# Kernel tuning notes

Hardware: AMD Instinct MI355X
Metric: run time of the kernel (lower is better)

Reference implementation:

```python
import jax, jax.numpy as jnp
import numpy as np

B, N, F, D, M, R, K, TOPR = 32, 1024, 10, 64, 4, 8, 20, 2
TAU = 1.0
BN_EPS = 1e-5


def setup_inputs() -> dict:
    key = jax.random.key(0)
    ks = jax.random.split(key, 20)
    s = 0.1
    p = {}
    p['data'] = jax.random.normal(ks[0], (B, N, F), jnp.float32)
    u = jnp.clip(jax.random.uniform(ks[1], (B, M), jnp.float32), 1e-6, 1.0 - 1e-6)
    p['gumbel_noise'] = -jnp.log(-jnp.log(u))
    p['W_cond'] = jax.random.normal(ks[2], (F, D), jnp.float32) * s
    p['b_cond'] = jnp.zeros((D,), jnp.float32)
    p['W_ap'] = jax.random.normal(ks[3], (D, D), jnp.float32) * s
    p['b_ap'] = jnp.zeros((D,), jnp.float32)
    p['W_av'] = jax.random.normal(ks[4], (D, 1), jnp.float32) * s
    p['W_r'] = jax.random.normal(ks[5], (D, M), jnp.float32) * s
    p['b_r'] = jnp.zeros((M,), jnp.float32)
    p['e_base'] = jax.random.normal(ks[6], (N, D), jnp.float32) * s
    p['lr_u'] = jax.random.normal(ks[7], (M, N, R), jnp.float32) * s
    p['lr_v'] = jax.random.normal(ks[8], (M, R, D), jnp.float32) * s
    p['W_gnn'] = jax.random.normal(ks[9], (F, D), jnp.float32) * s
    p['att_i'] = jax.random.normal(ks[10], (D,), jnp.float32) * s
    p['att_j'] = jax.random.normal(ks[11], (D,), jnp.float32) * s
    p['att_em_i'] = jax.random.normal(ks[12], (D,), jnp.float32) * s
    p['att_em_j'] = jax.random.normal(ks[13], (D,), jnp.float32) * s
    p['b_gnn'] = jnp.zeros((D,), jnp.float32)
    p['bn1_gamma'] = jnp.ones((D,), jnp.float32)
    p['bn1_beta'] = jnp.zeros((D,), jnp.float32)
    p['node_embed_table'] = jax.random.normal(ks[14], (N, D), jnp.float32) * s
    p['bn_out_gamma'] = jnp.ones((D,), jnp.float32)
    p['bn_out_beta'] = jnp.zeros((D,), jnp.float32)
    p['W_out'] = jax.random.normal(ks[15], (D, 1), jnp.float32) * s
    p['b_out'] = jnp.zeros((1,), jnp.float32)
    return p


def _nan(x):
    return jnp.nan_to_num(x, nan=0.0, posinf=1e4, neginf=-1e4)


def _bn(x, gamma, beta, axes):
    # BatchNorm1d in training mode: biased batch stats over `axes`.
    mu = x.mean(axes, keepdims=True)
    var = x.var(axes, keepdims=True)
    return (x - mu) * jax.lax.rsqrt(var + BN_EPS) * gamma + beta


def reference(data, gumbel_noise, W_cond, b_cond, W_ap, b_ap, W_av, W_r, b_r,
              e_base, lr_u, lr_v, W_gnn, att_i, att_j, att_em_i, att_em_j,
              b_gnn, bn1_gamma, bn1_beta, node_embed_table,
              bn_out_gamma, bn_out_beta, W_out, b_out):
    x_det = jax.lax.stop_gradient(data)                      # data.clone().detach()
    # --- condition attention pooling ---
    h_it = data @ W_cond + b_cond                            # [B,N,D]
    ah = jax.nn.leaky_relu(h_it @ W_ap + b_ap, 0.2)
    e_it = _nan((ah @ W_av)[..., 0])                         # [B,N]
    beta = jax.nn.softmax(e_it, axis=1)
    h_sys = jnp.sum(beta[..., None] * h_it, axis=1)          # [B,D]
    # --- gumbel top-k routing with straight-through ---
    pi_soft = jax.nn.softmax((h_sys @ W_r + b_r + gumbel_noise) / TAU, axis=-1)
    topv, topi = jax.lax.top_k(pi_soft, TOPR)
    pi_hard = jnp.sum(jax.nn.one_hot(topi, M, dtype=pi_soft.dtype) * topv[..., None], axis=1)
    pi_hard = pi_hard / jnp.maximum(pi_hard.sum(-1, keepdims=True), 1e-12)
    pi_t = jax.lax.stop_gradient(pi_hard - pi_soft) + pi_soft
    # --- low-rank expert prototypes -> mixed node embeddings ---
    proto = e_base[None] + jnp.einsum('mnr,mrd->mnd', lr_u, lr_v)    # [M,N,D]
    mixed = _nan(jnp.einsum('bm,mnd->bnd', pi_t, proto))             # [B,N,D]
    # --- dynamic top-k graph construction ---
    scores = _nan(jnp.einsum('bid,bjd->bij', mixed, mixed))          # [B,N,N]
    topk_vals, topk_idx = jax.lax.top_k(scores, K)                   # src nodes per dst: [B,N,K]
    topk_w = jax.nn.softmax(topk_vals, axis=-1)                      # edge weights
    # --- GAT-style layer with embedding-augmented keys, self loops re-added ---
    x_lin = x_det @ W_gnn                                            # [B,N,D]
    s_i = x_lin @ att_i + mixed @ att_em_i                           # [B,N]
    s_j = x_lin @ att_j + mixed @ att_em_j
    sj_nb = jnp.take_along_axis(s_j, topk_idx.reshape(B, N * K), axis=1).reshape(B, N, K)
    self_mask = topk_idx == jnp.arange(N)[None, :, None]             # remove_self_loops on topk edges
    alpha_nb = jnp.where(self_mask, -jnp.inf, jax.nn.leaky_relu(s_i[:, :, None] + sj_nb, 0.2))
    alpha_self = jax.nn.leaky_relu(s_i + s_j, 0.2)
    att = jax.nn.softmax(jnp.concatenate([alpha_nb, alpha_self[..., None]], axis=-1), axis=-1)
    w_nb = att[..., :K] * topk_w                                     # edge_weight modulation
    w_self = att[..., K]
    x_src = jnp.take_along_axis(x_lin, topk_idx.reshape(B, N * K)[..., None], axis=1).reshape(B, N, K, D)
    gnn = jnp.einsum('bnk,bnkd->bnd', w_nb, x_src) + w_self[..., None] * x_lin + b_gnn
    gnn = jax.nn.relu(_bn(gnn.reshape(B * N, D), bn1_gamma, bn1_beta, 0).reshape(B, N, D))
    # --- output head ---
    out = gnn * node_embed_table[None]                               # [B,N,D]
    out = jax.nn.relu(_bn(out, bn_out_gamma, bn_out_beta, (0, 1)))   # dropout = identity (eval)
    out = (out @ W_out + b_out).reshape(-1, N)                       # [B,N]
    return out, h_sys, pi_soft
```

## Files before the change

### kernel.cpp

```cpp
#include <hip/hip_runtime.h>
#include <math.h>

#define BB 32
#define NN 1024
#define FF 10
#define DD 64
#define MM 4
#define RR 8
#define KK 20
#define BNROWS (BB*NN)

#define OFF_HIT   0ull
#define OFF_XLIN  2097152ull
#define OFF_EIT   4194304ull
#define OFF_PIT   4227072ull
#define OFF_MIXED 4227200ull
#define OFF_SI    6324352ull
#define OFF_SJ    6357120ull
#define OFF_GNN   7700608ull
#define OFF_OUTP  9797760ull
#define OFF_STAT  11894912ull
#define OFF_SC    (OFF_STAT + 6464ull)

__device__ __forceinline__ float wave_sum(float v) {
    #pragma unroll
    for (int off = 32; off; off >>= 1) v += __shfl_xor(v, off);
    return v;
}
__device__ __forceinline__ float wave_max(float v) {
    #pragma unroll
    for (int off = 32; off; off >>= 1) v = fmaxf(v, __shfl_xor(v, off));
    return v;
}
__device__ __forceinline__ float lane_bcast(float v, int l) {
    return __int_as_float(__builtin_amdgcn_readlane(__float_as_int(v), l));
}

__global__ __launch_bounds__(256) void k_rows(
    const float* __restrict__ data, const float* __restrict__ W_cond,
    const float* __restrict__ b_cond, const float* __restrict__ W_ap,
    const float* __restrict__ b_ap, const float* __restrict__ W_av,
    const float* __restrict__ W_gnn,
    float* __restrict__ h_it, float* __restrict__ x_lin, float* __restrict__ e_it,
    float* __restrict__ stats)
{
    if (blockIdx.x < 26) {
        int idx = blockIdx.x * 256 + threadIdx.x;
        if (idx < 6432) stats[idx] = 0.f;
    }
    int w = threadIdx.x >> 6, lane = threadIdx.x & 63;
    int r = blockIdx.x * 4 + w;
    const float* dr = data + r * FF;
    float df[FF];
    #pragma unroll
    for (int f = 0; f < FF; f++) df[f] = dr[f];
    float h = b_cond[lane], x = 0.f;
    #pragma unroll
    for (int f = 0; f < FF; f++) {
        h = fmaf(df[f], W_cond[f * DD + lane], h);
        x = fmaf(df[f], W_gnn[f * DD + lane], x);
    }
    h_it[r * DD + lane] = h;
    x_lin[r * DD + lane] = x;
    float acc = b_ap[lane];
    #pragma unroll
    for (int e2 = 0; e2 < DD; e2++)
        acc = fmaf(lane_bcast(h, e2), W_ap[e2 * DD + lane], acc);
    float lr = acc > 0.f ? acc : 0.2f * acc;
    float ep = wave_sum(lr * W_av[lane]);
    if (lane == 0) e_it[r] = ep;
}

__global__ __launch_bounds__(256) void k_pool2(
    const float* __restrict__ e_it, const float* __restrict__ h_it,
    float* __restrict__ num, float* __restrict__ den)
{
    int w = threadIdx.x >> 6, lane = threadIdx.x & 63;
    int b = blockIdx.x >> 3, ch = blockIdx.x & 7;
    int base = b * NN + ch * 128 + w * 32;
    float acc = 0.f, dn = 0.f;
    #pragma unroll 4
    for (int i = 0; i < 32; i++) {
        float e = e_it[base + i];
        float wgt = expf(e);
        acc = fmaf(wgt, h_it[(size_t)(base + i) * DD + lane], acc);
        dn += wgt;
    }
    __shared__ float pa[4][DD];
    __shared__ float pd[4];
    pa[w][lane] = acc;
    if (lane == 0) pd[w] = dn;
    __syncthreads();
    if (w == 0) {
        float s = pa[0][lane] + pa[1][lane] + pa[2][lane] + pa[3][lane];
        atomicAdd(&num[b * DD + lane], s);
        if (lane == 0) atomicAdd(&den[b], pd[0] + pd[1] + pd[2] + pd[3]);
    }
}

__global__ void k_route(const float* __restrict__ num, const float* __restrict__ den,
                        const float* __restrict__ W_r, const float* __restrict__ b_r,
                        const float* __restrict__ gumbel,
                        float* __restrict__ h_sys, float* __restrict__ pi_soft,
                        float* __restrict__ pi_t)
{
    int tid = threadIdx.x;
    for (int i = tid; i < BB * DD; i += 256)
        h_sys[i] = num[i] / den[i >> 6];
    if (tid >= BB) return;
    int b = tid;
    float inv = 1.0f / den[b];
    float lg[MM];
    #pragma unroll
    for (int m = 0; m < MM; m++) lg[m] = b_r[m] + gumbel[b * MM + m];
    for (int d = 0; d < DD; d++) {
        float hv = num[b * DD + d] * inv;
        #pragma unroll
        for (int m = 0; m < MM; m++) lg[m] = fmaf(hv, W_r[d * MM + m], lg[m]);
    }
    float mx = fmaxf(fmaxf(lg[0], lg[1]), fmaxf(lg[2], lg[3]));
    float s = 0.f, p[MM];
    #pragma unroll
    for (int m = 0; m < MM; m++) { p[m] = expf(lg[m] - mx); s += p[m]; }
    #pragma unroll
    for (int m = 0; m < MM; m++) { p[m] /= s; pi_soft[b * MM + m] = p[m]; }
    int i1 = 0; float v1 = p[0];
    #pragma unroll
    for (int m = 1; m < MM; m++) if (p[m] > v1) { v1 = p[m]; i1 = m; }
    int i2 = -1; float v2 = -1.f;
    #pragma unroll
    for (int m = 0; m < MM; m++) if (m != i1 && p[m] > v2) { v2 = p[m]; i2 = m; }
    float norm = fmaxf(v1 + v2, 1e-12f);
    #pragma unroll
    for (int m = 0; m < MM; m++)
        pi_t[b * MM + m] = (m == i1 ? v1 : (m == i2 ? v2 : 0.f)) / norm;
}

__global__ __launch_bounds__(256) void k_mixed(
    const float* __restrict__ e_base, const float* __restrict__ lr_u,
    const float* __restrict__ lr_v, const float* __restrict__ pi_t,
    const float* __restrict__ x_lin,
    const float* __restrict__ att_i, const float* __restrict__ att_j,
    const float* __restrict__ att_em_i, const float* __restrict__ att_em_j,
    float* __restrict__ mixed, float* __restrict__ s_i, float* __restrict__ s_j)
{
    int w = threadIdx.x >> 6, lane = threadIdx.x & 63;
    int r = blockIdx.x * 4 + w;
    int b = r >> 10, n = r & 1023;
    float LR[MM];
    #pragma unroll
    for (int m = 0; m < MM; m++) {
        float a = 0.f;
        #pragma unroll
        for (int rr = 0; rr < RR; rr++)
            a = fmaf(lr_u[(m * NN + n) * RR + rr], lr_v[(m * RR + rr) * DD + lane], a);
        LR[m] = a;
    }
    float eb = e_base[n * DD + lane];
    float mx = 0.f;
    #pragma unroll
    for (int m = 0; m < MM; m++) mx = fmaf(pi_t[b * MM + m], eb + LR[m], mx);
    mixed[(size_t)r * DD + lane] = mx;
    float x = x_lin[(size_t)r * DD + lane];
    float r1 = wave_sum(x * att_i[lane] + mx * att_em_i[lane]);
    float r2 = wave_sum(x * att_j[lane] + mx * att_em_j[lane]);
    if (lane == 0) { s_i[r] = r1; s_j[r] = r2; }
}

__global__ __launch_bounds__(256) void k_score(
    const float* __restrict__ mixed_chunk, float* __restrict__ sc)
{
    __shared__ float As[32 * 132];
    __shared__ float Bs[32 * 132];
    int t = threadIdx.x;
    int bb = blockIdx.x >> 6;
    int rr = blockIdx.x & 63;
    int it = rr >> 3, jt = rr & 7;
    int i0 = it * 128, j0 = jt * 128;
    const float* mb = mixed_chunk + (size_t)bb * NN * DD;

    int tx = t & 15, ty = t >> 4;
    float acc[8][8];
    #pragma unroll
    for (int a = 0; a < 8; a++)
        #pragma unroll
        for (int bj = 0; bj < 8; bj++) acc[a][bj] = 0.f;

    int rowi[4], qi[4], swi[4];
    #pragma unroll
    for (int c = 0; c < 4; c++) {
        int id = t + c * 256;
        rowi[c] = (id & 15) | ((id >> 7) << 4);
        qi[c] = (id >> 4) & 7;
        swi[c] = ((rowi[c] & 4) << 4) | ((rowi[c] >> 3) << 2) | (rowi[c] & 3);
    }

    float4 pa[4], pb[4];
    #pragma unroll
    for (int c = 0; c < 4; c++) {
        pa[c] = *(const float4*)(mb + (size_t)(i0 + rowi[c]) * DD + qi[c] * 4);
        pb[c] = *(const float4*)(mb + (size_t)(j0 + rowi[c]) * DD + qi[c] * 4);
    }
    for (int hh = 0; hh < 2; hh++) {
        if (hh) __syncthreads();
        #pragma unroll
        for (int c = 0; c < 4; c++) {
            int pos = qi[c] * 4 * 132 + swi[c];
            As[pos] = pa[c].x; As[pos + 132] = pa[c].y; As[pos + 264] = pa[c].z; As[pos + 396] = pa[c].w;
            Bs[pos] = pb[c].x; Bs[pos + 132] = pb[c].y; Bs[pos + 264] = pb[c].z; Bs[pos + 396] = pb[c].w;
        }
        __syncthreads();
        if (hh == 0) {
            #pragma unroll
            for (int c = 0; c < 4; c++) {
                pa[c] = *(const float4*)(mb + (size_t)(i0 + rowi[c]) * DD + 32 + qi[c] * 4);
                pb[c] = *(const float4*)(mb + (size_t)(j0 + rowi[c]) * DD + 32 + qi[c] * 4);
            }
        }
        #pragma unroll 4
        for (int d = 0; d < 32; d++) {
            float4 a0 = *(const float4*)&As[d * 132 + ty * 4];
            float4 a1 = *(const float4*)&As[d * 132 + 64 + ty * 4];
            float4 b0 = *(const float4*)&Bs[d * 132 + tx * 4];
            float4 b1 = *(const float4*)&Bs[d * 132 + 64 + tx * 4];
            float av[8] = {a0.x, a0.y, a0.z, a0.w, a1.x, a1.y, a1.z, a1.w};
            float bv[8] = {b0.x, b0.y, b0.z, b0.w, b1.x, b1.y, b1.z, b1.w};
            #pragma unroll
            for (int a = 0; a < 8; a++)
                #pragma unroll
                for (int bj = 0; bj < 8; bj++)
                    acc[a][bj] = fmaf(av[a], bv[bj], acc[a][bj]);
        }
    }

    float* out = sc + ((size_t)bb * NN + i0 + ty * 8) * NN + j0 + tx * 8;
    #pragma unroll
    for (int a = 0; a < 8; a++) {
        float4 o0 = {acc[a][0], acc[a][1], acc[a][2], acc[a][3]};
        float4 o1 = {acc[a][4], acc[a][5], acc[a][6], acc[a][7]};
        *(float4*)(out + (size_t)a * NN) = o0;
        *(float4*)(out + (size_t)a * NN + 4) = o1;
    }
}

__global__ __launch_bounds__(256) void k_selgat(
    const float* __restrict__ sc, int b0,
    const float* __restrict__ x_lin, const float* __restrict__ s_i,
    const float* __restrict__ s_j, const float* __restrict__ b_gnn,
    float* __restrict__ gnn_pre, float* __restrict__ bstats)
{
    int w = threadIdx.x >> 6, lane = threadIdx.x & 63;
    int lr = blockIdx.x * 4 + w;
    int r = b0 * NN + lr;
    int b = r >> 10, n = r & 1023;
    const float* row = sc + (size_t)lr * NN;

    unsigned uk[16];
    #pragma unroll
    for (int c = 0; c < 4; c++) {
        float4 v = *(const float4*)(row + c * 256 + lane * 4);
        float vv[4] = {v.x, v.y, v.z, v.w};
        #pragma unroll
        for (int q = 0; q < 4; q++) {
            unsigned u = __float_as_uint(vv[q]);
            uk[c * 4 + q] = u ^ (((unsigned)((int)u >> 31)) | 0x80000000u);
        }
    }
    unsigned mx = uk[0];
    #pragma unroll
    for (int i = 1; i < 16; i++) mx = uk[i] > mx ? uk[i] : mx;
    unsigned sv = mx;
    #pragma unroll
    for (int blk = 2; blk <= 64; blk <<= 1) {
        #pragma unroll
        for (int dist = blk >> 1; dist >= 1; dist >>= 1) {
            unsigned pv = (unsigned)__shfl_xor((int)sv, dist);
            bool up = (lane & blk) == 0;
            bool upper = (lane & dist) == 0;
            bool g = sv > pv;
            sv = (((g == upper) == up)) ? sv : pv;
        }
    }
    unsigned tau = (unsigned)__shfl((int)sv, 19);

    __shared__ unsigned skey[4][64];
    __shared__ int sjj[4][64];
    int base = 0;
    #pragma unroll
    for (int s = 0; s < 16; s++) {
        bool q = uk[s] >= tau;
        unsigned long long m = __ballot(q);
        if (q) {
            int pos = base + __popcll(m & ((1ull << lane) - 1ull));
            if (pos < 64) {
                skey[w][pos] = uk[s];
                sjj[w][pos] = ((s >> 2) << 8) + lane * 4 + (s & 3);
            }
        }
        base += __popcll(m);
    }
    int C = base;

    float vk = -INFINITY; int ik = 0;
    if (C <= 64) {
        unsigned ck = 0u; int cj = 0x7FFFFFFF;
        if (lane < C) { ck = skey[w][lane]; cj = sjj[w][lane]; }
        if (C <= 32) {
            #pragma unroll
            for (int blk = 2; blk <= 32; blk <<= 1)
                #pragma unroll
                for (int dist = blk >> 1; dist >= 1; dist >>= 1) {
                    unsigned pk = (unsigned)__shfl_xor((int)ck, dist);
                    int pj = __shfl_xor(cj, dist);
                    bool up = (lane & blk) == 0;
                    bool upper = (lane & dist) == 0;
                    bool g = (ck > pk) || (ck == pk && cj < pj);
                    bool keep = ((g == upper) == up);
                    ck = keep ? ck : pk; cj = keep ? cj : pj;
                }
        } else {
            #pragma unroll
            for (int blk = 2; blk <= 64; blk <<= 1)
                #pragma unroll
                for (int dist = blk >> 1; dist >= 1; dist >>= 1) {
                    unsigned pk = (unsigned)__shfl_xor((int)ck, dist);
                    int pj = __shfl_xor(cj, dist);
                    bool up = (lane & blk) == 0;
                    bool upper = (lane & dist) == 0;
                    bool g = (ck > pk) || (ck == pk && cj < pj);
                    bool keep = ((g == upper) == up);
                    ck = keep ? ck : pk; cj = keep ? cj : pj;
                }
        }
        if (lane < KK) {
            unsigned u = (ck & 0x80000000u) ? (ck ^ 0x80000000u) : ~ck;
            vk = __uint_as_float(u);
            ik = cj;
        }
    } else {
        for (int k = 0; k < KK; k++) {
            unsigned bm = uk[0]; int bsl = 0;
            #pragma unroll
            for (int i = 1; i < 16; i++) if (uk[i] > bm) { bm = uk[i]; bsl = i; }
            unsigned wm = bm;
            #pragma unroll
            for (int off = 32; off; off >>= 1) {
                unsigned tt = (unsigned)__shfl_xor((int)wm, off);
                wm = tt > wm ? tt : wm;
            }
            unsigned long long ball = __ballot(bm == wm);
            int winner = (int)__builtin_ctzll(ball);
            int slotw = __shfl(bsl, winner);
            int jw = ((slotw >> 2) << 8) + winner * 4 + (slotw & 3);
            unsigned u2 = (wm & 0x80000000u) ? (wm ^ 0x80000000u) : ~wm;
            if (lane == k) { vk = __uint_as_float(u2); ik = jw; }
            if (lane == winner) uk[bsl] = 0u;
        }
    }

    float m1 = wave_max(vk);
    float ek = (lane < KK) ? expf(vk - m1) : 0.f;
    float s1v = wave_sum(ek);
    float wk = ek / s1v;
    float si = s_i[r], sjn = s_j[r];
    float a = -INFINITY;
    if (lane < KK) {
        float sjk = s_j[(b << 10) + ik];
        float t2 = si + sjk;
        a = (ik == n) ? -INFINITY : (t2 > 0.f ? t2 : 0.2f * t2);
    }
    float ts = si + sjn;
    float aself = ts > 0.f ? ts : 0.2f * ts;
    float am = wave_max(fmaxf(a, aself));
    float ea = (lane < KK && a != -INFINITY) ? expf(a - am) : 0.f;
    float es = expf(aself - am);
    float ssm = wave_sum(ea) + es;
    float wnb = (ea / ssm) * wk;
    float wself = es / ssm;
    float acc = b_gnn[lane] + wself * x_lin[(size_t)r * DD + lane];
    #pragma unroll
    for (int k = 0; k < KK; k++) {
        int jk = __shfl(ik, k);
        float wv = __shfl(wnb, k);
        acc = fmaf(wv, x_lin[((size_t)(b << 10) + jk) * DD + lane], acc);
    }
    gnn_pre[(size_t)r * DD + lane] = acc;

    __shared__ float ps[4][64], pq[4][64];
    ps[w][lane] = acc;
    pq[w][lane] = acc * acc;
    __syncthreads();
    if (w == 0) {
        float s = ps[0][lane] + ps[1][lane] + ps[2][lane] + ps[3][lane];
        float q2 = pq[0][lane] + pq[1][lane] + pq[2][lane] + pq[3][lane];
        float* bk = bstats + (size_t)(blockIdx.x & 31) * 128;
        atomicAdd(&bk[lane], s);
        atomicAdd(&bk[DD + lane], q2);
    }
}

__global__ __launch_bounds__(256) void k_bn1(
    const float* __restrict__ gnn_pre, float* __restrict__ stats,
    const float* __restrict__ bstats,
    const float* __restrict__ gamma, const float* __restrict__ beta,
    const float* __restrict__ net, float* __restrict__ out_pre)
{
    int tid = threadIdx.x;
    int d0 = (tid & 15) * 4;
    float mean4[4], rs4[4], bt4[4];
    #pragma unroll
    for (int k = 0; k < 4; k++) {
        float s = 0.f, q = 0.f;
        #pragma unroll 8
        for (int bk = 0; bk < 32; bk++) {
            s += bstats[bk * 128 + d0 + k];
            q += bstats[bk * 128 + 64 + d0 + k];
        }
        float mu = s * (1.0f / BNROWS);
        float var = q * (1.0f / BNROWS) - mu * mu;
        mean4[k] = mu;
        rs4[k] = rsqrtf(var + 1e-5f) * gamma[d0 + k];
        bt4[k] = beta[d0 + k];
    }
    float s4[4] = {0, 0, 0, 0}, q4[4] = {0, 0, 0, 0};
    size_t base4 = (size_t)blockIdx.x * 2048;
    #pragma unroll
    for (int i = 0; i < 8; i++) {
        size_t f4 = base4 + (size_t)i * 256 + tid;
        float4 v = ((const float4*)gnn_pre)[f4];
        int n = ((int)(f4 >> 4)) & 1023;
        float4 nv = ((const float4*)net)[(size_t)n * 16 + (tid & 15)];
        float vv[4] = {v.x, v.y, v.z, v.w};
        float nn2[4] = {nv.x, nv.y, nv.z, nv.w};
        float ov[4];
        #pragma unroll
        for (int k = 0; k < 4; k++) {
            float y = (vv[k] - mean4[k]) * rs4[k] + bt4[k];
            y = y > 0.f ? y : 0.f;
            float o = y * nn2[k];
            ov[k] = o;
            s4[k] += o;
            q4[k] = fmaf(o, o, q4[k]);
        }
        float4 o4 = {ov[0], ov[1], ov[2], ov[3]};
        ((float4*)out_pre)[f4] = o4;
    }
    __shared__ float4 ls[256], lq[256];
    ls[tid] = make_float4(s4[0], s4[1], s4[2], s4[3]);
    lq[tid] = make_float4(q4[0], q4[1], q4[2], q4[3]);
    __syncthreads();
    if (tid < 16) {
        float4 S = ls[tid], Q = lq[tid];
        #pragma unroll
        for (int rr = 1; rr < 16; rr++) {
            float4 a = ls[tid + 16 * rr], b = lq[tid + 16 * rr];
            S.x += a.x; S.y += a.y; S.z += a.z; S.w += a.w;
            Q.x += b.x; Q.y += b.y; Q.z += b.z; Q.w += b.w;
        }
        atomicAdd(&stats[128 + tid * 4 + 0], S.x);
        atomicAdd(&stats[128 + tid * 4 + 1], S.y);
        atomicAdd(&stats[128 + tid * 4 + 2], S.z);
        atomicAdd(&stats[128 + tid * 4 + 3], S.w);
        atomicAdd(&stats[192 + tid * 4 + 0], Q.x);
        atomicAdd(&stats[192 + tid * 4 + 1], Q.y);
        atomicAdd(&stats[192 + tid * 4 + 2], Q.z);
        atomicAdd(&stats[192 + tid * 4 + 3], Q.w);
    }
}

__global__ __launch_bounds__(256) void k_head(
    const float* __restrict__ out_pre, const float* __restrict__ stats,
    const float* __restrict__ gamma, const float* __restrict__ beta,
    const float* __restrict__ W_out, const float* __restrict__ b_out,
    float* __restrict__ out)
{
    int w = threadIdx.x >> 6, lane = threadIdx.x & 63;
    int r = blockIdx.x * 4 + w;
    float mean = stats[lane] * (1.0f / BNROWS);
    float var = stats[DD + lane] * (1.0f / BNROWS) - mean * mean;
    float rs = rsqrtf(var + 1e-5f);
    float y = (out_pre[(size_t)r * DD + lane] - mean) * rs * gamma[lane] + beta[lane];
    y = y > 0.f ? y : 0.f;
    float p = wave_sum(y * W_out[lane]);
    if (lane == 0) out[r] = p + b_out[0];
}

extern "C" void kernel_launch(void* const* d_in, const int* in_sizes, int n_in,
                              void* d_out, int out_size, void* d_ws, size_t ws_size,
                              hipStream_t stream)
{
    const float* data     = (const float*)d_in[0];
    const float* gumbel   = (const float*)d_in[1];
    const float* W_cond   = (const float*)d_in[2];
    const float* b_cond   = (const float*)d_in[3];
    const float* W_ap     = (const float*)d_in[4];
    const float* b_ap     = (const float*)d_in[5];
    const float* W_av     = (const float*)d_in[6];
    const float* W_r      = (const float*)d_in[7];
    const float* b_r      = (const float*)d_in[8];
    const float* e_base   = (const float*)d_in[9];
    const float* lr_u     = (const float*)d_in[10];
    const float* lr_v     = (const float*)d_in[11];
    const float* W_gnn    = (const float*)d_in[12];
    const float* att_i    = (const float*)d_in[13];
    const float* att_j    = (const float*)d_in[14];
    const float* att_em_i = (const float*)d_in[15];
    const float* att_em_j = (const float*)d_in[16];
    const float* b_gnn    = (const float*)d_in[17];
    const float* bn1_g    = (const float*)d_in[18];
    const float* bn1_b    = (const float*)d_in[19];
    const float* net      = (const float*)d_in[20];
    const float* bno_g    = (const float*)d_in[21];
    const float* bno_b    = (const float*)d_in[22];
    const float* W_out    = (const float*)d_in[23];
    const float* b_out    = (const float*)d_in[24];

    float* ws = (float*)d_ws;
    float* h_it   = ws + OFF_HIT;
    float* x_lin  = ws + OFF_XLIN;
    float* e_it   = ws + OFF_EIT;
    float* pi_t   = ws + OFF_PIT;
    float* mixed  = ws + OFF_MIXED;
    float* s_i    = ws + OFF_SI;
    float* s_j    = ws + OFF_SJ;
    float* gnn_pre = ws + OFF_GNN;
    float* out_pre = ws + OFF_OUTP;
    float* stats   = ws + OFF_STAT;
    float* bstats  = stats + 256;
    float* pnum    = stats + 4352;
    float* pden    = stats + 6400;

    float* out0    = (float*)d_out;
    float* h_sys   = out0 + BB * NN;
    float* pi_soft = out0 + BB * NN + BB * DD;

    k_rows<<<BNROWS / 4, 256, 0, stream>>>(data, W_cond, b_cond, W_ap, b_ap, W_av, W_gnn,
                                           h_it, x_lin, e_it, stats);
    k_pool2<<<BB * 8, 256, 0, stream>>>(e_it, h_it, pnum, pden);
    k_route<<<1, 256, 0, stream>>>(pnum, pden, W_r, b_r, gumbel, h_sys, pi_soft, pi_t);
    k_mixed<<<BNROWS / 4, 256, 0, stream>>>(e_base, lr_u, lr_v, pi_t, x_lin,
                                            att_i, att_j, att_em_i, att_em_j, mixed, s_i, s_j);

    size_t ws_floats = ws_size / 4;
    size_t avail = ws_floats > OFF_SC ? ws_floats - OFF_SC : 0;
    int cb = (int)(avail / (size_t)(NN * NN));
    if (cb > BB) cb = BB;
    float* sc = ws + OFF_SC;
    if (cb < 1) { cb = 2; sc = h_it; }
    for (int b0 = 0; b0 < BB; b0 += cb) {
        int c = (BB - b0) < cb ? (BB - b0) : cb;
        k_score<<<c * 64, 256, 0, stream>>>(mixed + (size_t)b0 * NN * DD, sc);
        k_selgat<<<c * 256, 256, 0, stream>>>(sc, b0, x_lin, s_i, s_j, b_gnn, gnn_pre, bstats);
    }

    k_bn1<<<256, 256, 0, stream>>>(gnn_pre, stats, bstats, bn1_g, bn1_b, net, out_pre);
    k_head<<<BNROWS / 4, 256, 0, stream>>>(out_pre, stats + 128, bno_g, bno_b, W_out, b_out, out0);
}
```

Measured before the change: 319.4 us.

## Replace bitonic sorts in top-k with radix-select threshold via ballots

```diff
diff --git a/kernel.cpp b/kernel.cpp
--- a/kernel.cpp
+++ b/kernel.cpp
@@ -269,19 +269,18 @@
     unsigned mx = uk[0];
     #pragma unroll
     for (int i = 1; i < 16; i++) mx = uk[i] > mx ? uk[i] : mx;
-    unsigned sv = mx;
-    #pragma unroll
-    for (int blk = 2; blk <= 64; blk <<= 1) {
-        #pragma unroll
-        for (int dist = blk >> 1; dist >= 1; dist >>= 1) {
-            unsigned pv = (unsigned)__shfl_xor((int)sv, dist);
-            bool up = (lane & blk) == 0;
-            bool upper = (lane & dist) == 0;
-            bool g = sv > pv;
-            sv = (((g == upper) == up)) ? sv : pv;
-        }
-    }
-    unsigned tau = (unsigned)__shfl((int)sv, 19);
+
+    unsigned tau = 0;
+    {
+        int need = KK;
+        for (int bb2 = 31; bb2 >= 0; --bb2) {
+            unsigned above = ~((2u << bb2) - 1u);
+            bool hit = ((mx & above) == tau) && ((mx >> bb2) & 1u);
+            int c1 = __popcll(__ballot(hit));
+            if (c1 >= need) tau |= (1u << bb2);
+            else need -= c1;
+        }
+    }
 
     __shared__ unsigned skey[4][64];
     __shared__ int sjj[4][64];
@@ -302,37 +301,39 @@
     int C = base;
 
     float vk = -INFINITY; int ik = 0;
+    bool issel = false;
     if (C <= 64) {
         unsigned ck = 0u; int cj = 0x7FFFFFFF;
         if (lane < C) { ck = skey[w][lane]; cj = sjj[w][lane]; }
-        if (C <= 32) {
-            #pragma unroll
-            for (int blk = 2; blk <= 32; blk <<= 1)
-                #pragma unroll
-                for (int dist = blk >> 1; dist >= 1; dist >>= 1) {
-                    unsigned pk = (unsigned)__shfl_xor((int)ck, dist);
-                    int pj = __shfl_xor(cj, dist);
-                    bool up = (lane & blk) == 0;
-                    bool upper = (lane & dist) == 0;
-                    bool g = (ck > pk) || (ck == pk && cj < pj);
-                    bool keep = ((g == upper) == up);
-                    ck = keep ? ck : pk; cj = keep ? cj : pj;
-                }
-        } else {
-            #pragma unroll
-            for (int blk = 2; blk <= 64; blk <<= 1)
-                #pragma unroll
-                for (int dist = blk >> 1; dist >= 1; dist >>= 1) {
-                    unsigned pk = (unsigned)__shfl_xor((int)ck, dist);
-                    int pj = __shfl_xor(cj, dist);
-                    bool up = (lane & blk) == 0;
-                    bool upper = (lane & dist) == 0;
-                    bool g = (ck > pk) || (ck == pk && cj < pj);
-                    bool keep = ((g == upper) == up);
-                    ck = keep ? ck : pk; cj = keep ? cj : pj;
-                }
-        }
-        if (lane < KK) {
+        unsigned tau2 = 0;
+        {
+            int need = KK;
+            for (int bb2 = 31; bb2 >= 0; --bb2) {
+                unsigned above = ~((2u << bb2) - 1u);
+                bool hit = ((ck & above) == tau2) && ((ck >> bb2) & 1u);
+                int c1 = __popcll(__ballot(hit));
+                if (c1 >= need) tau2 |= (1u << bb2);
+                else need -= c1;
+            }
+        }
+        bool isgt = ck > tau2;
+        int cntgt = __popcll(__ballot(isgt));
+        int needq = KK - cntgt;
+        bool iseq = (ck == tau2);
+        unsigned long long eqm = __ballot(iseq);
+        if (__popcll(eqm) > needq) {
+            unsigned pj = 0; int needs = needq;
+            for (int bb2 = 31; bb2 >= 0; --bb2) {
+                unsigned above = ~((2u << bb2) - 1u);
+                bool hit0 = iseq && (((unsigned)cj & above) == pj) && !(((unsigned)cj >> bb2) & 1u);
+                int c0 = __popcll(__ballot(hit0));
+                if (c0 >= needs) {  }
+                else { needs -= c0; pj |= (1u << bb2); }
+            }
+            iseq = iseq && ((unsigned)cj <= pj);
+        }
+        issel = isgt || iseq;
+        if (issel) {
             unsigned u = (ck & 0x80000000u) ? (ck ^ 0x80000000u) : ~ck;
             vk = __uint_as_float(u);
             ik = cj;
@@ -356,15 +357,16 @@
             if (lane == k) { vk = __uint_as_float(u2); ik = jw; }
             if (lane == winner) uk[bsl] = 0u;
         }
+        issel = (lane < KK);
     }
 
     float m1 = wave_max(vk);
-    float ek = (lane < KK) ? expf(vk - m1) : 0.f;
+    float ek = issel ? expf(vk - m1) : 0.f;
     float s1v = wave_sum(ek);
     float wk = ek / s1v;
     float si = s_i[r], sjn = s_j[r];
     float a = -INFINITY;
-    if (lane < KK) {
+    if (issel) {
         float sjk = s_j[(b << 10) + ik];
         float t2 = si + sjk;
         a = (ik == n) ? -INFINITY : (t2 > 0.f ? t2 : 0.2f * t2);
@@ -372,16 +374,19 @@
     float ts = si + sjn;
     float aself = ts > 0.f ? ts : 0.2f * ts;
     float am = wave_max(fmaxf(a, aself));
-    float ea = (lane < KK && a != -INFINITY) ? expf(a - am) : 0.f;
+    float ea = (issel && a != -INFINITY) ? expf(a - am) : 0.f;
     float es = expf(aself - am);
     float ssm = wave_sum(ea) + es;
     float wnb = (ea / ssm) * wk;
     float wself = es / ssm;
     float acc = b_gnn[lane] + wself * x_lin[(size_t)r * DD + lane];
-    #pragma unroll
+    unsigned long long selm = __ballot(issel);
+    #pragma unroll 1
     for (int k = 0; k < KK; k++) {
-        int jk = __shfl(ik, k);
-        float wv = __shfl(wnb, k);
+        int ln = (int)__builtin_ctzll(selm);
+        selm &= (selm - 1ull);
+        int jk = __builtin_amdgcn_readlane(ik, ln);
+        float wv = __int_as_float(__builtin_amdgcn_readlane(__float_as_int(wnb), ln));
         acc = fmaf(wv, x_lin[((size_t)(b << 10) + jk) * DD + lane], acc);
     }
     gnn_pre[(size_t)r * DD + lane] = acc;
```

Result: slower. 333.5 us (+4.4%).

## Fuse attention pooling and routing into row kernel with last-block reduction

Applied to the files above, without the earlier changes.

```diff
diff --git a/kernel.cpp b/kernel.cpp
--- a/kernel.cpp
+++ b/kernel.cpp
@@ -20,7 +20,7 @@
 #define OFF_GNN   7700608ull
 #define OFF_OUTP  9797760ull
 #define OFF_STAT  11894912ull
-#define OFF_SC    (OFF_STAT + 6464ull)
+#define OFF_SC    (OFF_STAT + 21008ull)
 
 __device__ __forceinline__ float wave_sum(float v) {
     #pragma unroll
@@ -40,16 +40,16 @@
     const float* __restrict__ data, const float* __restrict__ W_cond,
     const float* __restrict__ b_cond, const float* __restrict__ W_ap,
     const float* __restrict__ b_ap, const float* __restrict__ W_av,
-    const float* __restrict__ W_gnn,
-    float* __restrict__ h_it, float* __restrict__ x_lin, float* __restrict__ e_it,
-    float* __restrict__ stats)
-{
-    if (blockIdx.x < 26) {
-        int idx = blockIdx.x * 256 + threadIdx.x;
-        if (idx < 6432) stats[idx] = 0.f;
-    }
-    int w = threadIdx.x >> 6, lane = threadIdx.x & 63;
+    const float* __restrict__ W_gnn, const float* __restrict__ W_r,
+    const float* __restrict__ b_r, const float* __restrict__ gumbel,
+    float* __restrict__ x_lin,
+    float* pnumb, float* pdenb, unsigned* cnt,
+    float* __restrict__ h_sys, float* __restrict__ pi_soft, float* __restrict__ pi_t)
+{
+    int tid = threadIdx.x;
+    int w = tid >> 6, lane = tid & 63;
     int r = blockIdx.x * 4 + w;
+    int b = r >> 10;
     const float* dr = data + r * FF;
     float df[FF];
     #pragma unroll
@@ -60,61 +60,54 @@
         h = fmaf(df[f], W_cond[f * DD + lane], h);
         x = fmaf(df[f], W_gnn[f * DD + lane], x);
     }
-    h_it[r * DD + lane] = h;
-    x_lin[r * DD + lane] = x;
+    x_lin[(size_t)r * DD + lane] = x;
     float acc = b_ap[lane];
     #pragma unroll
     for (int e2 = 0; e2 < DD; e2++)
         acc = fmaf(lane_bcast(h, e2), W_ap[e2 * DD + lane], acc);
-    float lr = acc > 0.f ? acc : 0.2f * acc;
-    float ep = wave_sum(lr * W_av[lane]);
-    if (lane == 0) e_it[r] = ep;
-}
-
-__global__ __launch_bounds__(256) void k_pool2(
-    const float* __restrict__ e_it, const float* __restrict__ h_it,
-    float* __restrict__ num, float* __restrict__ den)
-{
-    int w = threadIdx.x >> 6, lane = threadIdx.x & 63;
-    int b = blockIdx.x >> 3, ch = blockIdx.x & 7;
-    int base = b * NN + ch * 128 + w * 32;
-    float acc = 0.f, dn = 0.f;
-    #pragma unroll 4
-    for (int i = 0; i < 32; i++) {
-        float e = e_it[base + i];
-        float wgt = expf(e);
-        acc = fmaf(wgt, h_it[(size_t)(base + i) * DD + lane], acc);
-        dn += wgt;
-    }
-    __shared__ float pa[4][DD];
-    __shared__ float pd[4];
-    pa[w][lane] = acc;
-    if (lane == 0) pd[w] = dn;
+    float lr2 = acc > 0.f ? acc : 0.2f * acc;
+    float ep = wave_sum(lr2 * W_av[lane]);
+    float wgt = expf(ep);
+    int bank = blockIdx.x & 7;
+    atomicAdd(&pnumb[bank * 2048 + b * 64 + lane], wgt * h);
+    if (lane == 0) atomicAdd(&pdenb[bank * 32 + b], wgt);
+
+    __shared__ int is_last;
     __syncthreads();
-    if (w == 0) {
-        float s = pa[0][lane] + pa[1][lane] + pa[2][lane] + pa[3][lane];
-        atomicAdd(&num[b * DD + lane], s);
-        if (lane == 0) atomicAdd(&den[b], pd[0] + pd[1] + pd[2] + pd[3]);
-    }
-}
-
-__global__ void k_route(const float* __restrict__ num, const float* __restrict__ den,
-                        const float* __restrict__ W_r, const float* __restrict__ b_r,
-                        const float* __restrict__ gumbel,
-                        float* __restrict__ h_sys, float* __restrict__ pi_soft,
-                        float* __restrict__ pi_t)
-{
-    int tid = threadIdx.x;
-    for (int i = tid; i < BB * DD; i += 256)
-        h_sys[i] = num[i] / den[i >> 6];
+    if (tid == 0) {
+        __threadfence();
+        unsigned old = atomicAdd(cnt, 1u);
+        is_last = (old == (unsigned)(gridDim.x - 1)) ? 1 : 0;
+    }
+    __syncthreads();
+    if (!is_last) return;
+    __threadfence();
+
+    __shared__ float den_s[BB];
+    if (tid < BB) {
+        float d2 = 0.f;
+        #pragma unroll
+        for (int bk = 0; bk < 8; bk++) d2 += pdenb[bk * 32 + tid];
+        den_s[tid] = d2;
+    }
+    __syncthreads();
+    for (int i = tid; i < BB * DD; i += 256) {
+        float s = 0.f;
+        #pragma unroll
+        for (int bk = 0; bk < 8; bk++) s += pnumb[bk * 2048 + i];
+        h_sys[i] = s / den_s[i >> 6];
+    }
     if (tid >= BB) return;
-    int b = tid;
-    float inv = 1.0f / den[b];
+    int bb = tid;
+    float inv = 1.0f / den_s[bb];
     float lg[MM];
     #pragma unroll
-    for (int m = 0; m < MM; m++) lg[m] = b_r[m] + gumbel[b * MM + m];
+    for (int m = 0; m < MM; m++) lg[m] = b_r[m] + gumbel[bb * MM + m];
     for (int d = 0; d < DD; d++) {
-        float hv = num[b * DD + d] * inv;
+        float s = 0.f;
+        #pragma unroll
+        for (int bk = 0; bk < 8; bk++) s += pnumb[bk * 2048 + bb * 64 + d];
+        float hv = s * inv;
         #pragma unroll
         for (int m = 0; m < MM; m++) lg[m] = fmaf(hv, W_r[d * MM + m], lg[m]);
     }
@@ -123,7 +116,7 @@
     #pragma unroll
     for (int m = 0; m < MM; m++) { p[m] = expf(lg[m] - mx); s += p[m]; }
     #pragma unroll
-    for (int m = 0; m < MM; m++) { p[m] /= s; pi_soft[b * MM + m] = p[m]; }
+    for (int m = 0; m < MM; m++) { p[m] /= s; pi_soft[bb * MM + m] = p[m]; }
     int i1 = 0; float v1 = p[0];
     #pragma unroll
     for (int m = 1; m < MM; m++) if (p[m] > v1) { v1 = p[m]; i1 = m; }
@@ -133,7 +126,7 @@
     float norm = fmaxf(v1 + v2, 1e-12f);
     #pragma unroll
     for (int m = 0; m < MM; m++)
-        pi_t[b * MM + m] = (m == i1 ? v1 : (m == i2 ? v2 : 0.f)) / norm;
+        pi_t[bb * MM + m] = (m == i1 ? v1 : (m == i2 ? v2 : 0.f)) / norm;
 }
 
 __global__ __launch_bounds__(256) void k_mixed(
@@ -516,10 +509,8 @@
     const float* b_out    = (const float*)d_in[24];
 
     float* ws = (float*)d_ws;
-    float* h_it   = ws + OFF_HIT;
     float* x_lin  = ws + OFF_XLIN;
-    float* e_it   = ws + OFF_EIT;
-    float* pi_t   = ws + OFF_PIT;
+    float* pi_tb  = ws + OFF_PIT;
     float* mixed  = ws + OFF_MIXED;
     float* s_i    = ws + OFF_SI;
     float* s_j    = ws + OFF_SJ;
@@ -527,18 +518,20 @@
     float* out_pre = ws + OFF_OUTP;
     float* stats   = ws + OFF_STAT;
     float* bstats  = stats + 256;
-    float* pnum    = stats + 4352;
-    float* pden    = stats + 6400;
+    float* pnumb   = stats + 4352;
+    float* pdenb   = stats + 20736;
+    unsigned* cnt  = (unsigned*)(stats + 20992);
 
     float* out0    = (float*)d_out;
     float* h_sys   = out0 + BB * NN;
     float* pi_soft = out0 + BB * NN + BB * DD;
 
+    hipMemsetAsync(stats, 0, 21000 * sizeof(float), stream);
+
     k_rows<<<BNROWS / 4, 256, 0, stream>>>(data, W_cond, b_cond, W_ap, b_ap, W_av, W_gnn,
-                                           h_it, x_lin, e_it, stats);
-    k_pool2<<<BB * 8, 256, 0, stream>>>(e_it, h_it, pnum, pden);
-    k_route<<<1, 256, 0, stream>>>(pnum, pden, W_r, b_r, gumbel, h_sys, pi_soft, pi_t);
-    k_mixed<<<BNROWS / 4, 256, 0, stream>>>(e_base, lr_u, lr_v, pi_t, x_lin,
+                                           W_r, b_r, gumbel, x_lin,
+                                           pnumb, pdenb, cnt, h_sys, pi_soft, pi_tb);
+    k_mixed<<<BNROWS / 4, 256, 0, stream>>>(e_base, lr_u, lr_v, pi_tb, x_lin,
                                             att_i, att_j, att_em_i, att_em_j, mixed, s_i, s_j);
 
     size_t ws_floats = ws_size / 4;
@@ -546,7 +539,7 @@
     int cb = (int)(avail / (size_t)(NN * NN));
     if (cb > BB) cb = BB;
     float* sc = ws + OFF_SC;
-    if (cb < 1) { cb = 2; sc = h_it; }
+    if (cb < 1) { cb = 2; sc = ws + OFF_HIT; }
     for (int b0 = 0; b0 < BB; b0 += cb) {
         int c = (BB - b0) < cb ? (BB - b0) : cb;
         k_score<<<c * 64, 256, 0, stream>>>(mixed + (size_t)b0 * NN * DD, sc);
```

Result: slower. 490.4 us (+53.5%).

## Retile score GEMM to 32x256 tiles with A rows read directly from global

Applied to the files above, without the earlier changes.

```diff
diff --git a/kernel.cpp b/kernel.cpp
--- a/kernel.cpp
+++ b/kernel.cpp
@@ -170,77 +170,69 @@
 __global__ __launch_bounds__(256) void k_score(
     const float* __restrict__ mixed_chunk, float* __restrict__ sc)
 {
-    __shared__ float As[32 * 132];
-    __shared__ float Bs[32 * 132];
+    __shared__ float BT[32 * 264];
     int t = threadIdx.x;
-    int bb = blockIdx.x >> 6;
-    int rr = blockIdx.x & 63;
-    int it = rr >> 3, jt = rr & 7;
-    int i0 = it * 128, j0 = jt * 128;
+    int w = t >> 6, lane = t & 63;
+    int bb = blockIdx.x >> 7;
+    int rr = blockIdx.x & 127;
+    int it = rr >> 2, jt = rr & 3;
+    int i0 = it * 32, j0 = jt * 256;
     const float* mb = mixed_chunk + (size_t)bb * NN * DD;
-
-    int tx = t & 15, ty = t >> 4;
-    float acc[8][8];
-    #pragma unroll
-    for (int a = 0; a < 8; a++)
-        #pragma unroll
-        for (int bj = 0; bj < 8; bj++) acc[a][bj] = 0.f;
-
-    int rowi[4], qi[4], swi[4];
-    #pragma unroll
-    for (int c = 0; c < 4; c++) {
-        int id = t + c * 256;
-        rowi[c] = (id & 15) | ((id >> 7) << 4);
-        qi[c] = (id >> 4) & 7;
-        swi[c] = ((rowi[c] & 4) << 4) | ((rowi[c] >> 3) << 2) | (rowi[c] & 3);
-    }
-
-    float4 pa[4], pb[4];
-    #pragma unroll
-    for (int c = 0; c < 4; c++) {
-        pa[c] = *(const float4*)(mb + (size_t)(i0 + rowi[c]) * DD + qi[c] * 4);
-        pb[c] = *(const float4*)(mb + (size_t)(j0 + rowi[c]) * DD + qi[c] * 4);
+    const float* arow = mb + (size_t)(i0 + w * 8) * DD;
+
+    float4 acc4[8];
+    #pragma unroll
+    for (int a = 0; a < 8; a++) acc4[a] = make_float4(0.f, 0.f, 0.f, 0.f);
+
+    float4 pf[8];
+    {
+        const float* src = mb + (size_t)(j0 + t) * DD;
+        #pragma unroll
+        for (int i = 0; i < 8; i++) pf[i] = *(const float4*)(src + i * 4);
     }
     for (int hh = 0; hh < 2; hh++) {
         if (hh) __syncthreads();
         #pragma unroll
-        for (int c = 0; c < 4; c++) {
-            int pos = qi[c] * 4 * 132 + swi[c];
-            As[pos] = pa[c].x; As[pos + 132] = pa[c].y; As[pos + 264] = pa[c].z; As[pos + 396] = pa[c].w;
-            Bs[pos] = pb[c].x; Bs[pos + 132] = pb[c].y; Bs[pos + 264] = pb[c].z; Bs[pos + 396] = pb[c].w;
+        for (int i = 0; i < 8; i++) {
+            float4 v = pf[i];
+            int d0 = i * 4;
+            BT[(d0 + 0) * 264 + t] = v.x;
+            BT[(d0 + 1) * 264 + t] = v.y;
+            BT[(d0 + 2) * 264 + t] = v.z;
+            BT[(d0 + 3) * 264 + t] = v.w;
         }
         __syncthreads();
         if (hh == 0) {
-            #pragma unroll
-            for (int c = 0; c < 4; c++) {
-                pa[c] = *(const float4*)(mb + (size_t)(i0 + rowi[c]) * DD + 32 + qi[c] * 4);
-                pb[c] = *(const float4*)(mb + (size_t)(j0 + rowi[c]) * DD + 32 + qi[c] * 4);
+            const float* src = mb + (size_t)(j0 + t) * DD + 32;
+            #pragma unroll
+            for (int i = 0; i < 8; i++) pf[i] = *(const float4*)(src + i * 4);
+        }
+        int dh = hh * 32;
+        #pragma unroll 2
+        for (int d4 = 0; d4 < 8; d4++) {
+            float4 av[8];
+            #pragma unroll
+            for (int a = 0; a < 8; a++)
+                av[a] = *(const float4*)(arow + (size_t)a * DD + dh + d4 * 4);
+            #pragma unroll
+            for (int dd = 0; dd < 4; dd++) {
+                float4 bv = *(const float4*)&BT[(d4 * 4 + dd) * 264 + lane * 4];
+                #pragma unroll
+                for (int a = 0; a < 8; a++) {
+                    float as = dd == 0 ? av[a].x : dd == 1 ? av[a].y : dd == 2 ? av[a].z : av[a].w;
+                    acc4[a].x = fmaf(as, bv.x, acc4[a].x);
+                    acc4[a].y = fmaf(as, bv.y, acc4[a].y);
+                    acc4[a].z = fmaf(as, bv.z, acc4[a].z);
+                    acc4[a].w = fmaf(as, bv.w, acc4[a].w);
+                }
             }
         }
-        #pragma unroll 4
-        for (int d = 0; d < 32; d++) {
-            float4 a0 = *(const float4*)&As[d * 132 + ty * 4];
-            float4 a1 = *(const float4*)&As[d * 132 + 64 + ty * 4];
-            float4 b0 = *(const float4*)&Bs[d * 132 + tx * 4];
-            float4 b1 = *(const float4*)&Bs[d * 132 + 64 + tx * 4];
-            float av[8] = {a0.x, a0.y, a0.z, a0.w, a1.x, a1.y, a1.z, a1.w};
-            float bv[8] = {b0.x, b0.y, b0.z, b0.w, b1.x, b1.y, b1.z, b1.w};
-            #pragma unroll
-            for (int a = 0; a < 8; a++)
-                #pragma unroll
-                for (int bj = 0; bj < 8; bj++)
-                    acc[a][bj] = fmaf(av[a], bv[bj], acc[a][bj]);
-        }
-    }
-
-    float* out = sc + ((size_t)bb * NN + i0 + ty * 8) * NN + j0 + tx * 8;
-    #pragma unroll
-    for (int a = 0; a < 8; a++) {
-        float4 o0 = {acc[a][0], acc[a][1], acc[a][2], acc[a][3]};
-        float4 o1 = {acc[a][4], acc[a][5], acc[a][6], acc[a][7]};
-        *(float4*)(out + (size_t)a * NN) = o0;
-        *(float4*)(out + (size_t)a * NN + 4) = o1;
-    }
+    }
+
+    float* out = sc + ((size_t)bb * NN + i0 + w * 8) * NN + j0 + lane * 4;
+    #pragma unroll
+    for (int a = 0; a < 8; a++)
+        *(float4*)(out + (size_t)a * NN) = acc4[a];
 }
 
 __global__ __launch_bounds__(256) void k_selgat(
@@ -549,7 +541,7 @@
     if (cb < 1) { cb = 2; sc = h_it; }
     for (int b0 = 0; b0 < BB; b0 += cb) {
         int c = (BB - b0) < cb ? (BB - b0) : cb;
-        k_score<<<c * 64, 256, 0, stream>>>(mixed + (size_t)b0 * NN * DD, sc);
+        k_score<<<c * 128, 256, 0, stream>>>(mixed + (size_t)b0 * NN * DD, sc);
         k_selgat<<<c * 256, 256, 0, stream>>>(sc, b0, x_lin, s_i, s_j, b_gnn, gnn_pre, bstats);
     }
 
```

New measurement: 358.5 us. 1.12x slower.
